# Kernel tuning notes

Measured on AMD Instinct MI355X. Metric: run time of the kernel, lower is better.

The kernel has to match this reference:

```python
import jax, jax.numpy as jnp
import numpy as np

B, D, E, H, L = 16384, 512, 16, 256, 64
NOISE_EPS = 0.01


def setup_inputs() -> dict:
    key = jax.random.key(0)
    ks = jax.random.split(key, 8)
    s = 0.05
    return {
        "x": jax.random.normal(ks[0], (B, D), dtype=jnp.float32),
        "noise": jax.random.normal(ks[1], (B, E), dtype=jnp.float32),
        "w_gate": jax.random.normal(ks[2], (D, E), dtype=jnp.float32) * s,
        "w_noise": jax.random.normal(ks[3], (D, E), dtype=jnp.float32) * s,
        "W1": jax.random.normal(ks[4], (E, D, H), dtype=jnp.float32) * s,
        "b1": jnp.zeros((E, H), dtype=jnp.float32),
        "W2": jax.random.normal(ks[5], (E, H, L), dtype=jnp.float32) * s,
        "b2": jnp.zeros((E, L), dtype=jnp.float32),
    }


def _noisy_gating(x, noise, w_gate, w_noise):
    clean_logits = x @ w_gate                                   # [B, E]
    noise_stddev = jax.nn.softplus(x @ w_noise) + NOISE_EPS     # [B, E]
    logits = jax.nn.softmax(clean_logits + noise * noise_stddev, axis=1)
    mean_weight = jnp.mean(logits, axis=-1) - 1e-8              # [B]
    gates = jnp.where(logits >= mean_weight[:, None], logits, 0.0)
    gates = gates / jnp.sum(gates, axis=-1, keepdims=True)
    return gates


def reference(x, noise, w_gate, w_noise, W1, b1, W2, b2):
    gates = _noisy_gating(x, noise, w_gate, w_noise)            # [B, E]
    # Dense equivalent of SparseDispatcher dispatch -> expert MLP -> combine:
    # combine scatters expert_e(x[b]) * gates[b,e] into slot (b, e), zeros elsewhere;
    # since gates==0 at masked slots, this equals gates[:,:,None] * all-expert outputs.
    h = jnp.tanh(jnp.einsum("bd,edh->beh", x, W1) + b1[None])   # [B, E, H]
    y = jnp.einsum("beh,ehl->bel", h, W2) + b2[None]            # [B, E, L]
    return gates[:, :, None] * y                                # [B, E, L]
```

## Files before the change

### kernel.cpp

```cpp
#include <hip/hip_runtime.h>
#include <stdint.h>

#define BROWS 16384
#define DDIM  512
#define EEXP  16
#define HDIM  256
#define LDIM  64
#define BM    64

typedef __bf16  bf16x8  __attribute__((ext_vector_type(8)));
typedef float   floatx4 __attribute__((ext_vector_type(4)));
typedef ushort  ushort8 __attribute__((ext_vector_type(8)));
typedef unsigned int u32;

__device__ __forceinline__ ushort f2bf(float f) {
    uint32_t u = __builtin_bit_cast(uint32_t, f);
    u += 0x7fffu + ((u >> 16) & 1u);
    return (ushort)(u >> 16);
}

__device__ __forceinline__ float fast_tanh(float x) {
    float e = __builtin_amdgcn_exp2f(x * 2.8853900817779268f);
    return 1.0f - 2.0f * __builtin_amdgcn_rcpf(e + 1.0f);
}

__device__ __forceinline__ void gl_lds16(const void* g, void* l) {
    __builtin_amdgcn_global_load_lds(
        (const __attribute__((address_space(1))) u32*)g,
        (__attribute__((address_space(3))) u32*)l, 16, 0, 0);
}

__global__ __launch_bounds__(256) void gating_kernel(
    const float* __restrict__ x,
    const float* __restrict__ noise,
    const float* __restrict__ wg,
    const float* __restrict__ wn,
    float* __restrict__ gates,
    ushort* __restrict__ xbf,
    u32* __restrict__ cntb,
    u32* __restrict__ rowtmp)
{
    __shared__ __align__(16) float xs[32 * 132];
    __shared__ __align__(16) float wTg[16 * 132];
    __shared__ __align__(16) float wTn[16 * 132];
    __shared__ u32 lcnt[16];
    __shared__ ushort lrows[16 * 32];

    const int t    = threadIdx.x;
    const int blk  = blockIdx.x;
    const int row0 = blk * 32;
    const int og   = t & 15, rg = t >> 4;

    if (t < 16) lcnt[t] = 0;

    floatx4 accg4[2] = {}, accn4[2] = {};

    for (int ch = 0; ch < 4; ++ch) {
        const int k0 = ch * 128;
        __syncthreads();
        {
            int r = t >> 3, c = (t & 7) * 16;
            const float* src = &x[(size_t)(row0 + r) * DDIM + k0 + c];
            float4 f[4];
            #pragma unroll
            for (int i = 0; i < 4; ++i)
                f[i] = reinterpret_cast<const float4*>(src)[i];
            float* dst = &xs[r * 132 + c];
            #pragma unroll
            for (int i = 0; i < 4; ++i)
                reinterpret_cast<float4*>(dst)[i] = f[i];

            const int row = row0 + r;
            const int sw  = r & 7;
            #pragma unroll
            for (int i = 0; i < 2; ++i) {
                int cb = k0 + c + i * 8;
                int kb = cb >> 6;
                int g  = (cb >> 3) & 7;
                int gp = g ^ sw;
                float4 a = f[i * 2], b = f[i * 2 + 1];
                ushort8 t8;
                t8[0]=f2bf(a.x); t8[1]=f2bf(a.y); t8[2]=f2bf(a.z); t8[3]=f2bf(a.w);
                t8[4]=f2bf(b.x); t8[5]=f2bf(b.y); t8[6]=f2bf(b.z); t8[7]=f2bf(b.w);
                *reinterpret_cast<ushort8*>(&xbf[(size_t)row * DDIM + kb * 64 + gp * 8]) = t8;
            }
        }
        {
            int d = t >> 1, e0 = (t & 1) * 8;
            float4 a0 = *reinterpret_cast<const float4*>(&wg[(size_t)(k0 + d) * EEXP + e0]);
            float4 a1 = *reinterpret_cast<const float4*>(&wg[(size_t)(k0 + d) * EEXP + e0 + 4]);
            float4 b0 = *reinterpret_cast<const float4*>(&wn[(size_t)(k0 + d) * EEXP + e0]);
            float4 b1 = *reinterpret_cast<const float4*>(&wn[(size_t)(k0 + d) * EEXP + e0 + 4]);
            wTg[(e0+0)*132+d]=a0.x; wTg[(e0+1)*132+d]=a0.y; wTg[(e0+2)*132+d]=a0.z; wTg[(e0+3)*132+d]=a0.w;
            wTg[(e0+4)*132+d]=a1.x; wTg[(e0+5)*132+d]=a1.y; wTg[(e0+6)*132+d]=a1.z; wTg[(e0+7)*132+d]=a1.w;
            wTn[(e0+0)*132+d]=b0.x; wTn[(e0+1)*132+d]=b0.y; wTn[(e0+2)*132+d]=b0.z; wTn[(e0+3)*132+d]=b0.w;
            wTn[(e0+4)*132+d]=b1.x; wTn[(e0+5)*132+d]=b1.y; wTn[(e0+6)*132+d]=b1.z; wTn[(e0+7)*132+d]=b1.w;
        }
        __syncthreads();

        #pragma unroll 8
        for (int d4 = 0; d4 < 32; ++d4) {
            floatx4 wgv = *reinterpret_cast<const floatx4*>(&wTg[og * 132 + d4 * 4]);
            floatx4 wnv = *reinterpret_cast<const floatx4*>(&wTn[og * 132 + d4 * 4]);
            #pragma unroll
            for (int rr = 0; rr < 2; ++rr) {
                floatx4 xv = *reinterpret_cast<const floatx4*>(&xs[(rg * 2 + rr) * 132 + d4 * 4]);
                accg4[rr] += xv * wgv;
                accn4[rr] += xv * wnv;
            }
        }
    }

    #pragma unroll
    for (int rr = 0; rr < 2; ++rr) {
        const int row = row0 + rg * 2 + rr;
        float accg = accg4[rr][0] + accg4[rr][1] + accg4[rr][2] + accg4[rr][3];
        float accn = accn4[rr][0] + accn4[rr][1] + accn4[rr][2] + accn4[rr][3];

        float sp = fmaxf(accn, 0.f) + log1pf(expf(-fabsf(accn)));
        float stddev = sp + 0.01f;
        float nz = noise[(size_t)row * EEXP + og];
        float z = accg + nz * stddev;

        float m = z;
        #pragma unroll
        for (int mask = 8; mask >= 1; mask >>= 1)
            m = fmaxf(m, __shfl_xor(m, mask, 16));
        float ez = expf(z - m);
        float s = ez;
        #pragma unroll
        for (int mask = 8; mask >= 1; mask >>= 1)
            s += __shfl_xor(s, mask, 16);
        float logit = ez / s;

        float lsum = logit;
        #pragma unroll
        for (int mask = 8; mask >= 1; mask >>= 1)
            lsum += __shfl_xor(lsum, mask, 16);
        float mean = lsum * (1.0f / 16.0f) - 1e-8f;

        float gate = (logit >= mean) ? logit : 0.0f;
        float denom = gate;
        #pragma unroll
        for (int mask = 8; mask >= 1; mask >>= 1)
            denom += __shfl_xor(denom, mask, 16);

        gates[(size_t)row * EEXP + og] = gate / denom;

        if (gate > 0.0f) {
            u32 p = atomicAdd(&lcnt[og], 1u);
            lrows[og * 32 + p] = (ushort)(rg * 2 + rr);
        }
    }

    __syncthreads();
    if (t < 16) cntb[t * 512 + blk] = lcnt[t];
    for (int i = t; i < 16 * 32; i += 256) {
        int e = i >> 5, j = i & 31;
        if ((u32)j < lcnt[e])
            rowtmp[(size_t)e * 16384 + blk * 32 + j] = row0 + lrows[e * 32 + j];
    }
}

__global__ __launch_bounds__(256) void compact_kernel(
    const u32* __restrict__ cntb,
    const u32* __restrict__ rowtmp,
    u32* __restrict__ rowlist,
    u32* __restrict__ cnt)
{
    __shared__ u32 base_s[16];
    const int b    = blockIdx.x;
    const int lane = threadIdx.x & 63;
    const int wave = threadIdx.x >> 6;

    for (int e = wave; e < 16; e += 4) {
        u32 s = 0;
        for (int i = lane; i < b; i += 64) s += cntb[e * 512 + i];
        #pragma unroll
        for (int off = 32; off; off >>= 1) s += __shfl_down(s, off, 64);
        if (lane == 0) {
            base_s[e] = s;
            if (b == 511) cnt[e] = s + cntb[e * 512 + 511];
        }
    }
    __syncthreads();

    const int t = threadIdx.x;
    for (int i = t; i < 512; i += 256) {
        int e = i >> 5, j = i & 31;
        if ((u32)j < cntb[e * 512 + b])
            rowlist[(size_t)e * BROWS + base_s[e] + j] =
                rowtmp[(size_t)e * 16384 + b * 32 + j];
    }
}

__global__ __launch_bounds__(256) void aux_kernel(
    const float* __restrict__ W1, ushort* __restrict__ W1T,
    const float* __restrict__ W2, ushort* __restrict__ W2T,
    const float* __restrict__ gates, float* __restrict__ out)
{
    int b = blockIdx.x;
    if (b >= 2304) {
        int i = (b - 2304) * 256 + threadIdx.x;
        int slot = i >> 4;
        if (gates[slot] == 0.0f) {
            float4 z = {0.f, 0.f, 0.f, 0.f};
            reinterpret_cast<float4*>(out)[i] = z;
        }
        return;
    }
    __shared__ float tile[32][33];
    const float* src; ushort* dst; int R, C, c0, r0, swz, ei;
    if (b < 2048) {
        ei = b >> 7; int rem = b & 127;
        c0 = (rem & 7) * 32; r0 = (rem >> 3) * 32;
        R = DDIM; C = HDIM; swz = 1;
        src = W1; dst = W1T;
    } else {
        b -= 2048;
        ei = b >> 4; int rem = b & 15;
        c0 = (rem & 1) * 32; r0 = (rem >> 1) * 32;
        R = HDIM; C = LDIM; swz = 0;
        src = W2; dst = W2T;
    }
    const int tx = threadIdx.x & 31, ty = threadIdx.x >> 5;
    const float* s = src + (size_t)ei * R * C;
    ushort* d = dst + (size_t)ei * R * C;

    #pragma unroll
    for (int i = 0; i < 4; ++i) {
        int rr = ty + i * 8;
        tile[rr][tx] = s[(size_t)(r0 + rr) * C + c0 + tx];
    }
    __syncthreads();
    #pragma unroll
    for (int i = 0; i < 4; ++i) {
        int cc = ty + i * 8;
        int h = c0 + cc;
        int col = r0 + tx;
        int col2 = col;
        if (swz) {
            int g = (col >> 3) & 7;
            col2 = (col & ~63) | ((g ^ (h & 7)) << 3) | (col & 7);
        }
        d[(size_t)h * R + col2] = f2bf(tile[tx][cc]);
    }
}

__global__ __launch_bounds__(256, 4) void expert_kernel(
    const ushort* __restrict__ xbf,
    const float*  __restrict__ gates,
    const ushort* __restrict__ W1T,
    const float*  __restrict__ b1,
    const ushort* __restrict__ W2T,
    const float*  __restrict__ b2,
    const u32*    __restrict__ cnt,
    const u32*    __restrict__ rowlist,
    float* __restrict__ out)
{
    __shared__ __align__(16) ushort lds[20480];

    const int bx = blockIdx.x;
    const int e  = bx & 15;
    const int t  = bx >> 4;

    const int count = (int)cnt[e];
    if (t * BM >= count) return;
    const int nrt = min(BM, count - t * BM);
    const u32* rl = rowlist + (size_t)e * BROWS + t * BM;

    const int tid  = threadIdx.x;
    const int lane = tid & 63;
    const int wave = tid >> 6;

    const int lr = lane & 15;
    const int q  = lane >> 4;
    const int kq = q * 8;
    const int rq = q * 4;
    const int la = lane >> 3, lb = lane & 7;

    const char* xg = (const char*)xbf;
    const char* w1 = (const char*)W1T + (size_t)e * HDIM * 1024;

    size_t abase[2]; int sxr[2];
    #pragma unroll
    for (int p = 0; p < 2; ++p) {
        int r  = wave * 16 + p * 8 + la;
        int rc = min(r, nrt - 1);
        u32 ri = rl[rc];
        abase[p] = (size_t)ri * 1024;
        sxr[p]   = (la ^ (int)(ri & 7)) << 4;
    }

    floatx4 acc[4][4] = {};

    for (int kb = 0; kb < 8; ++kb) {
        const int koff = kb * 128;
        #pragma unroll
        for (int p = 0; p < 2; ++p) {
            int c = wave * 2 + p;
            gl_lds16(xg + abase[p] + koff + ((lb << 4) ^ sxr[p]), &lds[c * 512]);
        }
        #pragma unroll
        for (int p = 0; p < 8; ++p) {
            int c = wave * 8 + p;
            gl_lds16(w1 + (size_t)(c * 8 + la) * 1024 + koff + (lb << 4),
                     &lds[4096 + c * 512]);
        }
        __syncthreads();

        #pragma unroll
        for (int s = 0; s < 2; ++s) {
            const int g = s * 4 + q;
            bf16x8 af[4], bfr[4];
            #pragma unroll
            for (int i = 0; i < 4; ++i) {
                int r = i * 16 + lr;
                af[i] = *reinterpret_cast<const bf16x8*>(&lds[r * 64 + ((g ^ (r & 7)) << 3)]);
            }
            #pragma unroll
            for (int j = 0; j < 4; ++j) {
                int r = wave * 64 + j * 16 + lr;
                bfr[j] = *reinterpret_cast<const bf16x8*>(&lds[4096 + r * 64 + ((g ^ (r & 7)) << 3)]);
            }
            #pragma unroll
            for (int i = 0; i < 4; ++i)
                #pragma unroll
                for (int j = 0; j < 4; ++j)
                    acc[i][j] = __builtin_amdgcn_mfma_f32_16x16x32_bf16(
                        af[i], bfr[j], acc[i][j], 0, 0, 0);
        }
        __syncthreads();
    }

    float b1v[4];
    #pragma unroll
    for (int j = 0; j < 4; ++j)
        b1v[j] = b1[e * HDIM + wave * 64 + j * 16 + lr];

    #pragma unroll
    for (int i = 0; i < 4; ++i)
        #pragma unroll
        for (int j = 0; j < 4; ++j) {
            int c = wave * 64 + j * 16 + lr;
            int gg = c >> 3;
            #pragma unroll
            for (int rr = 0; rr < 4; ++rr) {
                int r = i * 16 + rq + rr;
                float v = fast_tanh(acc[i][j][rr] + b1v[j]);
                lds[r * 256 + (((gg & 24) | ((gg & 7) ^ (r & 7))) << 3) + (c & 7)] = f2bf(v);
            }
        }
    __syncthreads();

    const ushort* w2 = W2T + (size_t)e * LDIM * HDIM;
    floatx4 acc2[4] = {};
    #pragma unroll
    for (int s = 0; s < 8; ++s) {
        int r = wave * 16 + lr;
        int g = s * 4 + q;
        bf16x8 af = *reinterpret_cast<const bf16x8*>(
            &lds[r * 256 + (((g & 24) | ((g & 7) ^ (r & 7))) << 3)]);
        #pragma unroll
        for (int j = 0; j < 4; ++j) {
            bf16x8 bfr = *reinterpret_cast<const bf16x8*>(
                &w2[(size_t)(j * 16 + lr) * HDIM + s * 32 + kq]);
            acc2[j] = __builtin_amdgcn_mfma_f32_16x16x32_bf16(af, bfr, acc2[j], 0, 0, 0);
        }
    }

    float b2v[4];
    #pragma unroll
    for (int j = 0; j < 4; ++j)
        b2v[j] = b2[e * LDIM + j * 16 + lr];

    #pragma unroll
    for (int rr = 0; rr < 4; ++rr) {
        int r  = wave * 16 + rq + rr;
        int rc = min(r, nrt - 1);
        u32 ri = rl[rc];
        float gsc = gates[(size_t)ri * EEXP + e];
        if (r < nrt) {
            #pragma unroll
            for (int j = 0; j < 4; ++j)
                out[(size_t)ri * (EEXP * LDIM) + e * LDIM + j * 16 + lr] =
                    (acc2[j][rr] + b2v[j]) * gsc;
        }
    }
}

extern "C" void kernel_launch(void* const* d_in, const int* in_sizes, int n_in,
                              void* d_out, int out_size, void* d_ws, size_t ws_size,
                              hipStream_t stream) {
    (void)in_sizes; (void)n_in; (void)out_size; (void)ws_size;
    const float* x     = (const float*)d_in[0];
    const float* noise = (const float*)d_in[1];
    const float* wg    = (const float*)d_in[2];
    const float* wn    = (const float*)d_in[3];
    const float* W1    = (const float*)d_in[4];
    const float* b1    = (const float*)d_in[5];
    const float* W2    = (const float*)d_in[6];
    const float* b2    = (const float*)d_in[7];
    float* out = (float*)d_out;

    char* ws = (char*)d_ws;
    float*  gates   = (float*)ws;
    ushort* W1T     = (ushort*)(ws + (1 << 20));
    ushort* W2T     = (ushort*)(ws + (5 << 20));
    ushort* xbf     = (ushort*)(ws + (6 << 20));
    u32*    cntb    = (u32*)(ws + (22 << 20));
    u32*    cnt     = (u32*)(ws + (22 << 20) + (32 << 10));
    u32*    rowtmp  = (u32*)(ws + (23 << 20));
    u32*    rowlist = (u32*)(ws + (24 << 20));

    gating_kernel<<<BROWS / 32, 256, 0, stream>>>(x, noise, wg, wn, gates, xbf, cntb, rowtmp);
    compact_kernel<<<512, 256, 0, stream>>>(cntb, rowtmp, rowlist, cnt);
    aux_kernel<<<2304 + 16384, 256, 0, stream>>>(W1, W1T, W2, W2T, gates, out);
    expert_kernel<<<(BROWS / BM) * EEXP, 256, 0, stream>>>(
        xbf, gates, W1T, b1, W2T, b2, cnt, rowlist, out);
}
```

Baseline: 185.5 us.

## Load W1 fragments directly into registers and double-buffer x tiles in LDS

The first expert GEMM no longer stages W1 through LDS. Each wave now reads its B fragments straight from global memory into registers, one step ahead with software prefetch, and the W1 transpose swizzle is removed to match. The x tile is double-buffered in LDS so the next k-block's copy overlaps the current MFMAs, which removes one barrier per iteration. LDS use drops, but register pressure rises, so occupancy is lowered from 4 to 3 blocks. Direct global loads of W1 may hit L2 less efficiently than the shared LDS tile did.

```diff
diff --git a/kernel.cpp b/kernel.cpp
--- a/kernel.cpp
+++ b/kernel.cpp
@@ -210,17 +210,17 @@
         return;
     }
     __shared__ float tile[32][33];
-    const float* src; ushort* dst; int R, C, c0, r0, swz, ei;
+    const float* src; ushort* dst; int R, C, c0, r0, ei;
     if (b < 2048) {
         ei = b >> 7; int rem = b & 127;
         c0 = (rem & 7) * 32; r0 = (rem >> 3) * 32;
-        R = DDIM; C = HDIM; swz = 1;
+        R = DDIM; C = HDIM;
         src = W1; dst = W1T;
     } else {
         b -= 2048;
         ei = b >> 4; int rem = b & 15;
         c0 = (rem & 1) * 32; r0 = (rem >> 1) * 32;
-        R = HDIM; C = LDIM; swz = 0;
+        R = HDIM; C = LDIM;
         src = W2; dst = W2T;
     }
     const int tx = threadIdx.x & 31, ty = threadIdx.x >> 5;
@@ -237,17 +237,11 @@
     for (int i = 0; i < 4; ++i) {
         int cc = ty + i * 8;
         int h = c0 + cc;
-        int col = r0 + tx;
-        int col2 = col;
-        if (swz) {
-            int g = (col >> 3) & 7;
-            col2 = (col & ~63) | ((g ^ (h & 7)) << 3) | (col & 7);
-        }
-        d[(size_t)h * R + col2] = f2bf(tile[tx][cc]);
-    }
-}
-
-__global__ __launch_bounds__(256, 4) void expert_kernel(
+        d[(size_t)h * R + r0 + tx] = f2bf(tile[tx][cc]);
+    }
+}
+
+__global__ __launch_bounds__(256, 3) void expert_kernel(
     const ushort* __restrict__ xbf,
     const float*  __restrict__ gates,
     const ushort* __restrict__ W1T,
@@ -258,7 +252,7 @@
     const u32*    __restrict__ rowlist,
     float* __restrict__ out)
 {
-    __shared__ __align__(16) ushort lds[20480];
+    __shared__ __align__(16) ushort lds[16384];
 
     const int bx = blockIdx.x;
     const int e  = bx & 15;
@@ -292,43 +286,63 @@
         sxr[p]   = (la ^ (int)(ri & 7)) << 4;
     }
 
+    const char* bptr[4];
+    #pragma unroll
+    for (int j = 0; j < 4; ++j)
+        bptr[j] = w1 + (size_t)(wave * 64 + j * 16 + lr) * 1024 + q * 16;
+
     floatx4 acc[4][4] = {};
 
+    bf16x8 bnx[4];
+    #pragma unroll
+    for (int j = 0; j < 4; ++j)
+        bnx[j] = *reinterpret_cast<const bf16x8*>(bptr[j]);
+
+    #pragma unroll
+    for (int p = 0; p < 2; ++p) {
+        int c = wave * 2 + p;
+        gl_lds16(xg + abase[p] + ((lb << 4) ^ sxr[p]), &lds[c * 512]);
+    }
+    __syncthreads();
+
+    #pragma unroll
     for (int kb = 0; kb < 8; ++kb) {
-        const int koff = kb * 128;
-        #pragma unroll
-        for (int p = 0; p < 2; ++p) {
-            int c = wave * 2 + p;
-            gl_lds16(xg + abase[p] + koff + ((lb << 4) ^ sxr[p]), &lds[c * 512]);
-        }
-        #pragma unroll
-        for (int p = 0; p < 8; ++p) {
-            int c = wave * 8 + p;
-            gl_lds16(w1 + (size_t)(c * 8 + la) * 1024 + koff + (lb << 4),
-                     &lds[4096 + c * 512]);
-        }
-        __syncthreads();
-
+        const int cur = (kb & 1) << 12;
+        if (kb < 7) {
+            const int koff = (kb + 1) * 128;
+            #pragma unroll
+            for (int p = 0; p < 2; ++p) {
+                int c = wave * 2 + p;
+                gl_lds16(xg + abase[p] + koff + ((lb << 4) ^ sxr[p]),
+                         &lds[(cur ^ 4096) + c * 512]);
+            }
+        }
         #pragma unroll
         for (int s = 0; s < 2; ++s) {
+            bf16x8 bc[4];
+            #pragma unroll
+            for (int j = 0; j < 4; ++j) bc[j] = bnx[j];
+            const int pn = kb * 2 + s + 1;
+            if (pn < 16) {
+                const int off = (pn >> 1) * 128 + (pn & 1) * 64;
+                #pragma unroll
+                for (int j = 0; j < 4; ++j)
+                    bnx[j] = *reinterpret_cast<const bf16x8*>(bptr[j] + off);
+            }
             const int g = s * 4 + q;
-            bf16x8 af[4], bfr[4];
+            bf16x8 af[4];
             #pragma unroll
             for (int i = 0; i < 4; ++i) {
                 int r = i * 16 + lr;
-                af[i] = *reinterpret_cast<const bf16x8*>(&lds[r * 64 + ((g ^ (r & 7)) << 3)]);
-            }
-            #pragma unroll
-            for (int j = 0; j < 4; ++j) {
-                int r = wave * 64 + j * 16 + lr;
-                bfr[j] = *reinterpret_cast<const bf16x8*>(&lds[4096 + r * 64 + ((g ^ (r & 7)) << 3)]);
+                af[i] = *reinterpret_cast<const bf16x8*>(
+                    &lds[cur + r * 64 + ((g ^ (r & 7)) << 3)]);
             }
             #pragma unroll
             for (int i = 0; i < 4; ++i)
                 #pragma unroll
                 for (int j = 0; j < 4; ++j)
                     acc[i][j] = __builtin_amdgcn_mfma_f32_16x16x32_bf16(
-                        af[i], bfr[j], acc[i][j], 0, 0, 0);
+                        af[i], bc[j], acc[i][j], 0, 0, 0);
         }
         __syncthreads();
     }
```

After: 196.3 us. +5.8%, slower.

## Double-buffer first GEMM K-loop with async prefetch and MFMA priority boost

Applied to the files above, without the earlier changes.

Converts the first expert GEMM loop into a two-stage pipeline: the LDS buffer is doubled, two K-tiles are prefetched up front, and each iteration waits with a partial vmcnt so the next tile's global-to-LDS loads overlap the current tile's MFMAs. It adds s_setprio around the MFMA block and replaces __syncthreads with explicit waitcnt plus barriers. The doubled LDS (80KB) forces launch bounds down from 4 to 2 blocks per CU, which lowers occupancy in exchange for overlap within each block.

```diff
diff --git a/kernel.cpp b/kernel.cpp
--- a/kernel.cpp
+++ b/kernel.cpp
@@ -247,7 +247,7 @@
     }
 }
 
-__global__ __launch_bounds__(256, 4) void expert_kernel(
+__global__ __launch_bounds__(256, 2) void expert_kernel(
     const ushort* __restrict__ xbf,
     const float*  __restrict__ gates,
     const ushort* __restrict__ W1T,
@@ -258,7 +258,7 @@
     const u32*    __restrict__ rowlist,
     float* __restrict__ out)
 {
-    __shared__ __align__(16) ushort lds[20480];
+    __shared__ __align__(16) ushort lds[40960];
 
     const int bx = blockIdx.x;
     const int e  = bx & 15;
@@ -292,23 +292,37 @@
         sxr[p]   = (la ^ (int)(ri & 7)) << 4;
     }
 
-    floatx4 acc[4][4] = {};
-
-    for (int kb = 0; kb < 8; ++kb) {
-        const int koff = kb * 128;
+    auto stage = [&](int tl) {
+        const int koff = tl * 128;
+        const int da = (tl & 1) << 12;
+        const int db = 8192 + ((tl & 1) << 14);
         #pragma unroll
         for (int p = 0; p < 2; ++p) {
             int c = wave * 2 + p;
-            gl_lds16(xg + abase[p] + koff + ((lb << 4) ^ sxr[p]), &lds[c * 512]);
+            gl_lds16(xg + abase[p] + koff + ((lb << 4) ^ sxr[p]), &lds[da + c * 512]);
         }
         #pragma unroll
         for (int p = 0; p < 8; ++p) {
             int c = wave * 8 + p;
             gl_lds16(w1 + (size_t)(c * 8 + la) * 1024 + koff + (lb << 4),
-                     &lds[4096 + c * 512]);
-        }
-        __syncthreads();
-
+                     &lds[db + c * 512]);
+        }
+    };
+
+    floatx4 acc[4][4] = {};
+
+    stage(0);
+    stage(1);
+
+    #pragma unroll
+    for (int kb = 0; kb < 8; ++kb) {
+        if (kb < 7) { asm volatile("s_waitcnt vmcnt(10)" ::: "memory"); }
+        else        { asm volatile("s_waitcnt vmcnt(0)"  ::: "memory"); }
+        __builtin_amdgcn_s_barrier();
+        __builtin_amdgcn_sched_barrier(0);
+
+        const int cA = (kb & 1) << 12;
+        const int cB = 8192 + ((kb & 1) << 14);
         #pragma unroll
         for (int s = 0; s < 2; ++s) {
             const int g = s * 4 + q;
@@ -316,21 +330,28 @@
             #pragma unroll
             for (int i = 0; i < 4; ++i) {
                 int r = i * 16 + lr;
-                af[i] = *reinterpret_cast<const bf16x8*>(&lds[r * 64 + ((g ^ (r & 7)) << 3)]);
+                af[i] = *reinterpret_cast<const bf16x8*>(
+                    &lds[cA + r * 64 + ((g ^ (r & 7)) << 3)]);
             }
             #pragma unroll
             for (int j = 0; j < 4; ++j) {
                 int r = wave * 64 + j * 16 + lr;
-                bfr[j] = *reinterpret_cast<const bf16x8*>(&lds[4096 + r * 64 + ((g ^ (r & 7)) << 3)]);
+                bfr[j] = *reinterpret_cast<const bf16x8*>(
+                    &lds[cB + r * 64 + ((g ^ (r & 7)) << 3)]);
             }
+            __builtin_amdgcn_s_setprio(1);
             #pragma unroll
             for (int i = 0; i < 4; ++i)
                 #pragma unroll
                 for (int j = 0; j < 4; ++j)
                     acc[i][j] = __builtin_amdgcn_mfma_f32_16x16x32_bf16(
                         af[i], bfr[j], acc[i][j], 0, 0, 0);
-        }
-        __syncthreads();
+            __builtin_amdgcn_s_setprio(0);
+        }
+        asm volatile("s_waitcnt lgkmcnt(0)" ::: "memory");
+        __builtin_amdgcn_s_barrier();
+        __builtin_amdgcn_sched_barrier(0);
+        if (kb < 6) stage(kb + 2);
     }
 
     float b1v[4];
```

Result: no change. 185.1 us (-0.2%).

## Fuse gating, compaction and weight transpose into one launch with atomic row lists

Applied to the files above, without the earlier changes.

Merges the gating, compaction and weight-transpose kernels into a single launch. Extra blocks do the W1/W2 bf16 transpose, and gating blocks reserve per-expert row-list slots with a global atomicAdd in place of a separate prefix-sum kernel. Zeroing of masked output slots moves into the gating threads, which now write zeros directly instead of a separate pass re-reading gates. This removes two kernel launches and the intermediate count and row-tmp buffers, at the cost of a memset and nondeterministic row order within each expert list.

```diff
diff --git a/kernel.cpp b/kernel.cpp
--- a/kernel.cpp
+++ b/kernel.cpp
@@ -30,20 +30,67 @@
         (__attribute__((address_space(3))) u32*)l, 16, 0, 0);
 }
 
-__global__ __launch_bounds__(256) void gating_kernel(
+__global__ __launch_bounds__(256) void gate_aux_kernel(
     const float* __restrict__ x,
     const float* __restrict__ noise,
     const float* __restrict__ wg,
     const float* __restrict__ wn,
+    const float* __restrict__ W1,
+    const float* __restrict__ W2,
     float* __restrict__ gates,
     ushort* __restrict__ xbf,
-    u32* __restrict__ cntb,
-    u32* __restrict__ rowtmp)
+    ushort* __restrict__ W1T,
+    ushort* __restrict__ W2T,
+    u32* __restrict__ cnt,
+    u32* __restrict__ rowlist,
+    float* __restrict__ out)
 {
+    if (blockIdx.x >= 512) {
+        __shared__ float tile[32][33];
+        int b = blockIdx.x - 512;
+        const float* src; ushort* dst; int R, C, c0, r0, swz, ei;
+        if (b < 2048) {
+            ei = b >> 7; int rem = b & 127;
+            c0 = (rem & 7) * 32; r0 = (rem >> 3) * 32;
+            R = DDIM; C = HDIM; swz = 1;
+            src = W1; dst = W1T;
+        } else {
+            b -= 2048;
+            ei = b >> 4; int rem = b & 15;
+            c0 = (rem & 1) * 32; r0 = (rem >> 1) * 32;
+            R = HDIM; C = LDIM; swz = 0;
+            src = W2; dst = W2T;
+        }
+        const int tx = threadIdx.x & 31, ty = threadIdx.x >> 5;
+        const float* s = src + (size_t)ei * R * C;
+        ushort* d = dst + (size_t)ei * R * C;
+
+        #pragma unroll
+        for (int i = 0; i < 4; ++i) {
+            int rr = ty + i * 8;
+            tile[rr][tx] = s[(size_t)(r0 + rr) * C + c0 + tx];
+        }
+        __syncthreads();
+        #pragma unroll
+        for (int i = 0; i < 4; ++i) {
+            int cc = ty + i * 8;
+            int h = c0 + cc;
+            int col = r0 + tx;
+            int col2 = col;
+            if (swz) {
+                int g = (col >> 3) & 7;
+                col2 = (col & ~63) | ((g ^ (h & 7)) << 3) | (col & 7);
+            }
+            d[(size_t)h * R + col2] = f2bf(tile[tx][cc]);
+        }
+        return;
+    }
+
     __shared__ __align__(16) float xs[32 * 132];
     __shared__ __align__(16) float wTg[16 * 132];
     __shared__ __align__(16) float wTn[16 * 132];
     __shared__ u32 lcnt[16];
+    __shared__ u32 lbase[16];
     __shared__ ushort lrows[16 * 32];
 
     const int t    = threadIdx.x;
@@ -150,100 +197,22 @@
         if (gate > 0.0f) {
             u32 p = atomicAdd(&lcnt[og], 1u);
             lrows[og * 32 + p] = (ushort)(rg * 2 + rr);
+        } else {
+            float4 zf = {0.f, 0.f, 0.f, 0.f};
+            float4* o = reinterpret_cast<float4*>(
+                &out[(size_t)row * (EEXP * LDIM) + og * LDIM]);
+            #pragma unroll
+            for (int i = 0; i < 16; ++i) o[i] = zf;
         }
     }
 
     __syncthreads();
-    if (t < 16) cntb[t * 512 + blk] = lcnt[t];
+    if (t < 16) lbase[t] = atomicAdd(&cnt[t], lcnt[t]);
+    __syncthreads();
     for (int i = t; i < 16 * 32; i += 256) {
         int e = i >> 5, j = i & 31;
         if ((u32)j < lcnt[e])
-            rowtmp[(size_t)e * 16384 + blk * 32 + j] = row0 + lrows[e * 32 + j];
-    }
-}
-
-__global__ __launch_bounds__(256) void compact_kernel(
-    const u32* __restrict__ cntb,
-    const u32* __restrict__ rowtmp,
-    u32* __restrict__ rowlist,
-    u32* __restrict__ cnt)
-{
-    __shared__ u32 base_s[16];
-    const int b    = blockIdx.x;
-    const int lane = threadIdx.x & 63;
-    const int wave = threadIdx.x >> 6;
-
-    for (int e = wave; e < 16; e += 4) {
-        u32 s = 0;
-        for (int i = lane; i < b; i += 64) s += cntb[e * 512 + i];
-        #pragma unroll
-        for (int off = 32; off; off >>= 1) s += __shfl_down(s, off, 64);
-        if (lane == 0) {
-            base_s[e] = s;
-            if (b == 511) cnt[e] = s + cntb[e * 512 + 511];
-        }
-    }
-    __syncthreads();
-
-    const int t = threadIdx.x;
-    for (int i = t; i < 512; i += 256) {
-        int e = i >> 5, j = i & 31;
-        if ((u32)j < cntb[e * 512 + b])
-            rowlist[(size_t)e * BROWS + base_s[e] + j] =
-                rowtmp[(size_t)e * 16384 + b * 32 + j];
-    }
-}
-
-__global__ __launch_bounds__(256) void aux_kernel(
-    const float* __restrict__ W1, ushort* __restrict__ W1T,
-    const float* __restrict__ W2, ushort* __restrict__ W2T,
-    const float* __restrict__ gates, float* __restrict__ out)
-{
-    int b = blockIdx.x;
-    if (b >= 2304) {
-        int i = (b - 2304) * 256 + threadIdx.x;
-        int slot = i >> 4;
-        if (gates[slot] == 0.0f) {
-            float4 z = {0.f, 0.f, 0.f, 0.f};
-            reinterpret_cast<float4*>(out)[i] = z;
-        }
-        return;
-    }
-    __shared__ float tile[32][33];
-    const float* src; ushort* dst; int R, C, c0, r0, swz, ei;
-    if (b < 2048) {
-        ei = b >> 7; int rem = b & 127;
-        c0 = (rem & 7) * 32; r0 = (rem >> 3) * 32;
-        R = DDIM; C = HDIM; swz = 1;
-        src = W1; dst = W1T;
-    } else {
-        b -= 2048;
-        ei = b >> 4; int rem = b & 15;
-        c0 = (rem & 1) * 32; r0 = (rem >> 1) * 32;
-        R = HDIM; C = LDIM; swz = 0;
-        src = W2; dst = W2T;
-    }
-    const int tx = threadIdx.x & 31, ty = threadIdx.x >> 5;
-    const float* s = src + (size_t)ei * R * C;
-    ushort* d = dst + (size_t)ei * R * C;
-
-    #pragma unroll
-    for (int i = 0; i < 4; ++i) {
-        int rr = ty + i * 8;
-        tile[rr][tx] = s[(size_t)(r0 + rr) * C + c0 + tx];
-    }
-    __syncthreads();
-    #pragma unroll
-    for (int i = 0; i < 4; ++i) {
-        int cc = ty + i * 8;
-        int h = c0 + cc;
-        int col = r0 + tx;
-        int col2 = col;
-        if (swz) {
-            int g = (col >> 3) & 7;
-            col2 = (col & ~63) | ((g ^ (h & 7)) << 3) | (col & 7);
-        }
-        d[(size_t)h * R + col2] = f2bf(tile[tx][cc]);
+            rowlist[(size_t)e * BROWS + lbase[e] + j] = row0 + lrows[e * 32 + j];
     }
 }
 
@@ -408,14 +377,12 @@
     ushort* W1T     = (ushort*)(ws + (1 << 20));
     ushort* W2T     = (ushort*)(ws + (5 << 20));
     ushort* xbf     = (ushort*)(ws + (6 << 20));
-    u32*    cntb    = (u32*)(ws + (22 << 20));
-    u32*    cnt     = (u32*)(ws + (22 << 20) + (32 << 10));
-    u32*    rowtmp  = (u32*)(ws + (23 << 20));
+    u32*    cnt     = (u32*)(ws + (22 << 20));
     u32*    rowlist = (u32*)(ws + (24 << 20));
 
-    gating_kernel<<<BROWS / 32, 256, 0, stream>>>(x, noise, wg, wn, gates, xbf, cntb, rowtmp);
-    compact_kernel<<<512, 256, 0, stream>>>(cntb, rowtmp, rowlist, cnt);
-    aux_kernel<<<2304 + 16384, 256, 0, stream>>>(W1, W1T, W2, W2T, gates, out);
+    hipMemsetAsync(cnt, 0, EEXP * sizeof(u32), stream);
+    gate_aux_kernel<<<512 + 2304, 256, 0, stream>>>(
+        x, noise, wg, wn, W1, W2, gates, xbf, W1T, W2T, cnt, rowlist, out);
     expert_kernel<<<(BROWS / BM) * EEXP, 256, 0, stream>>>(
         xbf, gates, W1T, b1, W2T, b2, cnt, rowlist, out);
 }
```

Result: faster. 177.2 us (-4.4%).
